# Kernel optimization log

Hardware: AMD Instinct MI355X
Metric: run time of the kernel (lower is better)

The kernel has to match this reference:

```python
import jax, jax.numpy as jnp
import numpy as np

NUM_WIRES = 14
N_LAYERS = 4
BATCH = 128


def _rx_mat(theta):
    # PennyLane RX(t) = [[cos(t/2), -i sin(t/2)], [-i sin(t/2), cos(t/2)]]
    c = jnp.cos(theta / 2).astype(jnp.complex64)
    s = jnp.sin(theta / 2).astype(jnp.complex64)
    row0 = jnp.stack([c, -1j * s], axis=-1)
    row1 = jnp.stack([-1j * s, c], axis=-1)
    return jnp.stack([row0, row1], axis=-2)  # (..., 2, 2)


def _rz_mat(theta):
    # PennyLane RZ(t) = diag(exp(-it/2), exp(it/2))
    e0 = jnp.exp(-1j * theta.astype(jnp.complex64) / 2)
    e1 = jnp.exp(1j * theta.astype(jnp.complex64) / 2)
    z = jnp.zeros_like(e0)
    row0 = jnp.stack([e0, z], axis=-1)
    row1 = jnp.stack([z, e1], axis=-1)
    return jnp.stack([row0, row1], axis=-2)


def _apply_1q(psi, gate, wire):
    # psi: (B, 2, 2, ..., 2); gate: (2,2) shared or (B,2,2) per-sample
    axis = wire + 1
    psi = jnp.moveaxis(psi, axis, -1)
    if gate.ndim == 2:
        psi = psi @ gate.T
    else:
        psi = jnp.einsum('b...j,bij->b...i', psi, gate)
    return jnp.moveaxis(psi, -1, axis)


def _apply_cnot(psi, ctrl, tgt):
    ac, at = ctrl + 1, tgt + 1
    psi0 = jnp.take(psi, 0, axis=ac)
    psi1 = jnp.take(psi, 1, axis=ac)
    at_adj = at - (1 if at > ac else 0)  # target axis shifts after removing ctrl axis
    psi1 = jnp.flip(psi1, axis=at_adj)   # X on target when ctrl=1
    return jnp.stack([psi0, psi1], axis=ac)


def _circuit(x, weights):
    # x: (B, n) real angles; weights: (L, n, 2)
    B = x.shape[0]
    n = NUM_WIRES
    psi = jnp.zeros((B,) + (2,) * n, jnp.complex64)
    psi = psi.at[(slice(None),) + (0,) * n].set(1.0)  # |0...0>
    # data encoding: per-sample RX gates
    for i in range(n):
        psi = _apply_1q(psi, _rx_mat(x[:, i]), i)
    # variational ansatz
    for l in range(N_LAYERS):
        for i in range(n):
            psi = _apply_1q(psi, _rx_mat(weights[l, i, 0]), i)
            psi = _apply_1q(psi, _rz_mat(weights[l, i, 1]), i)
        for i in range(n - 1):
            psi = _apply_cnot(psi, i, i + 1)
        psi = _apply_cnot(psi, n - 1, 0)
    # <Z_i> for every wire
    p = jnp.abs(psi) ** 2  # (B, 2, ..., 2) real
    zs = []
    for i in range(n):
        other = tuple(a for a in range(1, n + 1) if a != i + 1)
        m = jnp.sum(p, axis=other)  # (B, 2)
        zs.append(m[:, 0] - m[:, 1])
    return jnp.stack(zs, axis=-1)  # (B, n)


def setup_inputs() -> dict:
    key = jax.random.key(0)
    k1, k2, k3, k4 = jax.random.split(key, 4)
    states = jax.random.normal(k1, (BATCH, 2 ** NUM_WIRES), dtype=jnp.float32)
    weights = jax.random.normal(k2, (N_LAYERS, NUM_WIRES, 2), dtype=jnp.float32)
    lim = 1.0 / np.sqrt(NUM_WIRES)
    head_w = jax.random.uniform(k3, (1, NUM_WIRES), jnp.float32, -lim, lim)
    head_b = jax.random.uniform(k4, (1,), jnp.float32, -lim, lim)
    return {"states": states, "weights": weights, "head_w": head_w, "head_b": head_b}


def reference(states, weights, head_w, head_b):
    features = jnp.abs(states)[:, :NUM_WIRES]        # (B, n)
    qfeatures = _circuit(features, weights)          # (B, n)
    out = (qfeatures @ head_w.T + head_b)[:, 0]      # (B,)
    return out
```

## Files before the change

kernel.cpp:

```cpp
#include <hip/hip_runtime.h>
#include <math.h>

#define NW 14
#define NSTATE 16384
#define HALF 8192
#define NL 4
#define BATCH 128
#define TPB 1024
#define SHB1 (84 * 1024)
#define SHB2 ((NSTATE + 3 * TPB) * (int)sizeof(float2))


#define B4_  0x201Fu
#define B5_  0x203Fu
#define B12_ 0x3FFFu
#define B13_ 0x1FFFu

#define WAVE_FENCE() __builtin_amdgcn_wave_barrier()

__device__ __forceinline__ unsigned sxmap(unsigned v) {
    unsigned t = v;
    t ^= t >> 1; t ^= t >> 2; t ^= t >> 4; t ^= t >> 8;
    return (t & 0x0FFFu) | ((t & 1u) << 13);
}

__device__ __forceinline__ float2 cmul(float2 u, float2 v) {
    return make_float2(u.x * v.x - u.y * v.y, u.x * v.y + u.y * v.x);
}

__device__ __forceinline__ float4 fused_coef(const float* weights,
                                             const float* states,
                                             int b, int l, int w) {
    float t1 = weights[(l * NW + w) * 2 + 0];
    float t2 = weights[(l * NW + w) * 2 + 1];
    if (l == 0) t1 += fabsf(states[(size_t)b * NSTATE + w]);
    float s, c, sz, cz;
    sincosf(0.5f * t1, &s, &c);
    sincosf(0.5f * t2, &sz, &cz);
    return make_float4(c * cz, -c * sz, -s * sz, -s * cz);
}

template<int N, int M>
__device__ __forceinline__ void gateN(float2* r, float4 g, unsigned s3) {
    const float f = (s3 & (unsigned)M) ? -1.0f : 1.0f;
    g.y *= f;
    g.z *= f;
#pragma unroll
    for (int k = 0; k < N; ++k) {
        if ((k & M) == 0) {
            const float x0 = r[k].x,   y0 = r[k].y;
            const float x1 = r[k|M].x, y1 = r[k|M].y;
            r[k].x   =  g.x*x0 - g.y*y0 + g.z*x1 - g.w*y1;
            r[k].y   =  g.x*y0 + g.y*x0 + g.z*y1 + g.w*x1;
            r[k|M].x = -g.z*x0 - g.w*y0 + g.x*x1 + g.y*y1;
            r[k|M].y = -g.z*y0 + g.w*x0 + g.x*y1 - g.y*x1;
        }
    }
}

template<int J0, int S3SH, int S3MSK>
__device__ __forceinline__ void pass3h(float2* psi, const float4* gc,
                                       unsigned t) {
    const float4 gA = gc[13 - (J0 + 0)];
    const float4 gB = gc[13 - (J0 + 1)];
    const float4 gC = gc[13 - (J0 + 2)];
    const unsigned s3   = (t >> S3SH) & (unsigned)S3MSK;
    const unsigned low  = t & ((1u << J0) - 1u);
    const unsigned high = (t >> J0) << (J0 + 3);
    float2 r[8];
#pragma unroll
    for (int k = 0; k < 8; ++k)
        r[k] = psi[low | (((unsigned)k ^ s3) << J0) | high];
    gateN<8,1>(r, gA, s3);
    gateN<8,2>(r, gB, s3);
    gateN<8,4>(r, gC, s3);
#pragma unroll
    for (int k = 0; k < 8; ++k)
        psi[low | (((unsigned)k ^ s3) << J0) | high] = r[k];
}

template<int J0, int S3SH, int S3MSK>
__device__ __forceinline__ void pass3f(float2* psi, const float4* gc,
                                       unsigned t) {
    const float4 gA = gc[13 - (J0 + 0)];
    const float4 gB = gc[13 - (J0 + 1)];
    const float4 gC = gc[13 - (J0 + 2)];
    const unsigned s3 = (t >> S3SH) & (unsigned)S3MSK;
#pragma unroll
    for (int m = 0; m < 2; ++m) {
        const unsigned x    = t | ((unsigned)m << 10);
        const unsigned low  = x & ((1u << J0) - 1u);
        const unsigned high = (x >> J0) << (J0 + 3);
        float2 r[8];
#pragma unroll
        for (int k = 0; k < 8; ++k)
            r[k] = psi[low | (((unsigned)k ^ s3) << J0) | high];
        gateN<8,1>(r, gA, s3);
        gateN<8,2>(r, gB, s3);
        gateN<8,4>(r, gC, s3);
#pragma unroll
        for (int k = 0; k < 8; ++k)
            psi[low | (((unsigned)k ^ s3) << J0) | high] = r[k];
    }
}

__device__ __forceinline__ void passE(float2* psi, float2* spare,
                                      const float4* gc4, int l, unsigned t) {
    const float4 g1 = gc4[l*NW + 1];
    const float4 g0 = gc4[l*NW + 0];

    unsigned v = t;
    v ^= v >> 1; v ^= v >> 2; v ^= v >> 4; v ^= v >> 8;
    const unsigned Rinv0 = (v & 0x0FFFu) | ((v & 1u) << 13);

    float2 c0[4];
#pragma unroll
    for (int k = 0; k < 4; ++k) c0[k] = psi[t | ((unsigned)k << 12)];
    gateN<4,1>(c0, g1, 0u);
    gateN<4,2>(c0, g0, 0u);
    spare[3*t+0] = c0[1];
    spare[3*t+1] = c0[2];
    spare[3*t+2] = c0[3];
    const float2 keep = c0[0];

    float2 r[12];
#pragma unroll
    for (int m = 1; m < 4; ++m) {
        const unsigned base = t | ((unsigned)m << 10);
#pragma unroll
        for (int k = 0; k < 4; ++k)
            r[(m-1)*4 + k] = psi[base | ((unsigned)k << 12)];
    }
#pragma unroll
    for (int m = 0; m < 3; ++m) {
        gateN<4,1>(r + 4*m, g1, 0u);
        gateN<4,2>(r + 4*m, g0, 0u);
    }

    __syncthreads();

#pragma unroll
    for (int m = 1; m < 4; ++m) {
        const unsigned Rb = Rinv0 ^ ((m & 1) ? 0x27FFu : 0u)
                                  ^ ((m & 2) ? 0x2FFFu : 0u);
#pragma unroll
        for (int k = 0; k < 4; ++k) {
            const unsigned CK = ((k & 1) ? B12_ : 0u) ^ ((k & 2) ? B13_ : 0u);
            psi[Rb ^ CK] = r[(m-1)*4 + k];
        }
    }
    psi[Rinv0]           = keep;
    psi[Rinv0 ^ B12_]    = spare[3*t+0];
    psi[Rinv0 ^ B13_]    = spare[3*t+1];
    psi[Rinv0 ^ 0x2000u] = spare[3*t+2];
}

__device__ __forceinline__ void exit_scatter(const float2* psi,
                                             float2* __restrict__ dst,
                                             float4 g1, unsigned q,
                                             unsigned tid) {
#pragma unroll
    for (int m = 0; m < 4; ++m) {
        const unsigned jc = tid + (unsigned)m * TPB;
        const float2 x0 = psi[jc];
        const float2 x1 = psi[jc | 0x1000u];
        float2 A0, A1;
        A0.x =  g1.x*x0.x - g1.y*x0.y + g1.z*x1.x - g1.w*x1.y;
        A0.y =  g1.x*x0.y + g1.y*x0.x + g1.z*x1.y + g1.w*x1.x;
        A1.x = -g1.z*x0.x - g1.w*x0.y + g1.x*x1.x + g1.y*x1.y;
        A1.y = -g1.z*x0.y + g1.w*x0.x + g1.x*x1.y - g1.y*x1.x;
        const unsigned d0 = sxmap(jc) ^ (q ? 0x1FFFu : 0u);
        dst[d0]           = A0;
        dst[d0 ^ 0x3FFFu] = A1;
    }
}

__global__ __launch_bounds__(TPB) void k_layer1(
    const float* __restrict__ states, const float* __restrict__ weights,
    float2* __restrict__ Sout)
{
    extern __shared__ float2 psi[];
    __shared__ float2 vfac[NW][2];
    __shared__ float2 T1[128];
    __shared__ float2 T2[128];
    __shared__ float4 gc[NW];
    const unsigned gid = blockIdx.x, q = gid >> 7, b = gid & 127u;
    const unsigned tid = threadIdx.x;

    if (tid < NW) {
        float4 g = fused_coef(weights, states, (int)b, 0, (int)tid);
        vfac[tid][0] = make_float2(g.x, g.y);
        vfac[tid][1] = make_float2(-g.z, g.w);
    }
    if (tid >= 64 && tid < 64 + NW)
        gc[tid - 64] = fused_coef(weights, states, (int)b, 1, (int)(tid - 64));
    __syncthreads();
    if (tid < 128) {
        float2 p = make_float2(1.0f, 0.0f);
#pragma unroll
        for (int j = 0; j < 7; ++j)
            p = cmul(p, vfac[13 - j][(tid >> j) & 1u]);
        T1[tid] = p;
    } else if (tid < 256) {
        const unsigned u = tid - 128;
        float2 p = make_float2(1.0f, 0.0f);
#pragma unroll
        for (int j = 7; j < 14; ++j)
            p = cmul(p, vfac[13 - j][(u >> (j - 7)) & 1u]);
        T2[u] = p;
    }
    __syncthreads();

#pragma unroll
    for (int m = 0; m < 8; ++m) {
        const unsigned I  = tid + (unsigned)m * TPB;
        const unsigned If = I | (q << 13);
        const unsigned lo  = (If ^ (If >> 1)) & 0x0FFFu;
        const unsigned y12 = ((If >> 12) ^ (If >> 13) ^ If) & 1u;
        const unsigned y13 = ((If >> 13) ^ If) & 1u;
        const unsigned J = lo | (y12 << 12) | (y13 << 13);
        psi[I] = cmul(T1[J & 127u], T2[J >> 7]);
    }
    __syncthreads();

    pass3h<0, 1, 7>(psi, gc, tid);  WAVE_FENCE();
    pass3h<3, 3, 1>(psi, gc, tid);  WAVE_FENCE();
    pass3h<6, 0, 0>(psi, gc, tid);  __syncthreads();
    pass3h<9, 0, 0>(psi, gc, tid);  __syncthreads();

    exit_scatter(psi, Sout + (size_t)b * NSTATE, gc[1], q, tid);
}

__global__ __launch_bounds__(TPB) void k_rest(
    const float* __restrict__ states, const float* __restrict__ weights,
    const float* __restrict__ head_w, const float* __restrict__ head_b,
    const float2* __restrict__ Sin, float* __restrict__ out)
{
    extern __shared__ float2 dyn[];
    float2* psi   = dyn;
    float2* spare = dyn + NSTATE;
    __shared__ float4 gc4[NL * NW];
    __shared__ float wsum[TPB / 64];
    const unsigned b = blockIdx.x;
    const unsigned tid = threadIdx.x;

    if (tid < NL * NW)
        gc4[tid] = fused_coef(weights, states, (int)b,
                              (int)tid / NW, (int)tid % NW);
    __syncthreads();

    {
        const float4 ge = gc4[1 * NW + 0];
#pragma unroll
        for (int qm = 0; qm < 8; ++qm) {
            const unsigned q = (unsigned)qm >> 2;
            const unsigned m = (unsigned)qm & 3u;
            const float2* src = Sin + (size_t)b * NSTATE + (size_t)q * HALF;
            const unsigned ic = tid + m * TPB;
            const float2 f0 = src[ic];
            const float2 f1 = src[ic ^ 0x1FFFu];
            const unsigned rc = (q ^ ic) & 1u;
            const float aar = ge.x, aai = rc ? -ge.y : ge.y;
            const float bbr = rc ? -ge.z : ge.z, bbi = ge.w;
            float2 oc, op;
            oc.x = aar*f0.x - aai*f0.y + bbr*f1.x - bbi*f1.y;
            oc.y = aar*f0.y + aai*f0.x + bbr*f1.y + bbi*f1.x;
            op.x = aar*f1.x + aai*f1.y - (bbr*f0.x + bbi*f0.y);
            op.y = aar*f1.y - aai*f1.x - (bbr*f0.y - bbi*f0.x);
            psi[(q << 13) | ic]            = oc;
            psi[(q << 13) | (ic ^ 0x1FFFu)] = op;
        }
    }
    __syncthreads();

    pass3f<0, 1, 7>(psi, gc4 + 2 * NW, tid);  WAVE_FENCE();
    pass3f<3, 3, 1>(psi, gc4 + 2 * NW, tid);  WAVE_FENCE();
    pass3f<6, 0, 0>(psi, gc4 + 2 * NW, tid);  __syncthreads();
    pass3f<9, 0, 0>(psi, gc4 + 2 * NW, tid);  __syncthreads();
    passE(psi, spare, gc4, 2, tid);           __syncthreads();

    pass3f<0, 1, 7>(psi, gc4 + 3 * NW, tid);  WAVE_FENCE();
    pass3f<3, 3, 1>(psi, gc4 + 3 * NW, tid);  WAVE_FENCE();
    pass3f<6, 0, 0>(psi, gc4 + 3 * NW, tid);  __syncthreads();
    pass3f<9, 0, 0>(psi, gc4 + 3 * NW, tid);  __syncthreads();

    float hw[NW];
#pragma unroll
    for (int i = 0; i < NW; ++i) hw[i] = head_w[i];
    float H = 0.0f, H12 = 0.0f;
#pragma unroll
    for (int i = 0; i < NW; ++i) H += hw[i];
#pragma unroll
    for (int i = 2; i < NW; ++i) H12 += hw[i];

    const float4 g1 = gc4[3 * NW + 1];
    const float4 g0 = gc4[3 * NW + 0];

    float acc = 0.0f;
#pragma unroll
    for (int m2 = 0; m2 < 4; ++m2) {
        const unsigned base = tid | ((unsigned)m2 << 10);
        float2 r[4];
#pragma unroll
        for (int k = 0; k < 4; ++k)
            r[k] = psi[base | ((unsigned)k << 12)];
        gateN<4,1>(r, g1, 0u);
        gateN<4,2>(r, g0, 0u);
        float A = 0.0f;
        unsigned sfx = 0u;
#pragma unroll
        for (int p = 11; p >= 0; --p) {
            sfx ^= (base >> p) & 1u;
            if (sfx) A += hw[13 - p];
        }
        const unsigned P = sfx;
#pragma unroll
        for (int k = 0; k < 4; ++k) {
            const unsigned u   = ((unsigned)k ^ ((unsigned)k >> 1)) & 1u;
            const unsigned b13 = P ^ ((unsigned)k & 1u);
            float sum = u ? (H12 - A) : A;
            if (u)   sum += hw[1];
            if (b13) sum += hw[0];
            const float cv = H - 2.0f * sum;
            acc += (r[k].x * r[k].x + r[k].y * r[k].y) * cv;
        }
    }
#pragma unroll
    for (int off = 32; off > 0; off >>= 1)
        acc += __shfl_down(acc, off, 64);
    if ((tid & 63u) == 0) wsum[tid >> 6] = acc;
    __syncthreads();
    if (tid == 0) {
        float tot = 0.0f;
#pragma unroll
        for (int i = 0; i < TPB / 64; ++i) tot += wsum[i];
        out[b] = tot + head_b[0];
    }
}

extern "C" void kernel_launch(void* const* d_in, const int* in_sizes, int n_in,
                              void* d_out, int out_size, void* d_ws, size_t ws_size,
                              hipStream_t stream) {
    const float* states  = (const float*)d_in[0];
    const float* weights = (const float*)d_in[1];
    const float* head_w  = (const float*)d_in[2];
    const float* head_b  = (const float*)d_in[3];
    float* out = (float*)d_out;

    float2* SA = (float2*)d_ws;

    k_layer1<<<2 * BATCH, TPB, SHB1, stream>>>(states, weights, SA);
    k_rest  <<<BATCH, TPB, SHB2, stream>>>(states, weights, head_w, head_b,
                                           SA, out);
}
```

Before: 101.1 us.

## Fuse four qubit gates per LDS pass to cut passes and barriers

Replaces the 3-qubit-per-pass shared-memory sweeps (four passes per layer, each thread doing two 8-element groups) with 4-qubit passes. Each thread now loads 16 amplitudes once and applies four gates, so there are three passes per layer and fewer block barriers. Only the first pass keeps an XOR swizzle to avoid bank conflicts. The cost is more registers per thread (16 complex values), which may reduce occupancy, and bank conflicts in the unswizzled passes may change.

```diff
diff --git a/kernel.cpp b/kernel.cpp
--- a/kernel.cpp
+++ b/kernel.cpp
@@ -11,8 +11,6 @@
 #define SHB2 ((NSTATE + 3 * TPB) * (int)sizeof(float2))
 
 
-#define B4_  0x201Fu
-#define B5_  0x203Fu
 #define B12_ 0x3FFFu
 #define B13_ 0x1FFFu
 
@@ -79,29 +77,27 @@
         psi[low | (((unsigned)k ^ s3) << J0) | high] = r[k];
 }
 
-template<int J0, int S3SH, int S3MSK>
-__device__ __forceinline__ void pass3f(float2* psi, const float4* gc,
+template<int J0, bool SWZ>
+__device__ __forceinline__ void pass4f(float2* psi, const float4* gc,
                                        unsigned t) {
     const float4 gA = gc[13 - (J0 + 0)];
     const float4 gB = gc[13 - (J0 + 1)];
     const float4 gC = gc[13 - (J0 + 2)];
-    const unsigned s3 = (t >> S3SH) & (unsigned)S3MSK;
-#pragma unroll
-    for (int m = 0; m < 2; ++m) {
-        const unsigned x    = t | ((unsigned)m << 10);
-        const unsigned low  = x & ((1u << J0) - 1u);
-        const unsigned high = (x >> J0) << (J0 + 3);
-        float2 r[8];
-#pragma unroll
-        for (int k = 0; k < 8; ++k)
-            r[k] = psi[low | (((unsigned)k ^ s3) << J0) | high];
-        gateN<8,1>(r, gA, s3);
-        gateN<8,2>(r, gB, s3);
-        gateN<8,4>(r, gC, s3);
-#pragma unroll
-        for (int k = 0; k < 8; ++k)
-            psi[low | (((unsigned)k ^ s3) << J0) | high] = r[k];
-    }
+    const float4 gD = gc[13 - (J0 + 3)];
+    const unsigned s    = SWZ ? (t & 15u) : 0u;
+    const unsigned low  = t & ((1u << J0) - 1u);
+    const unsigned high = (t >> J0) << (J0 + 4);
+    float2 r[16];
+#pragma unroll
+    for (int k = 0; k < 16; ++k)
+        r[k] = psi[low | (((unsigned)k ^ s) << J0) | high];
+    gateN<16,1>(r, gA, s);
+    gateN<16,2>(r, gB, s);
+    gateN<16,4>(r, gC, s);
+    gateN<16,8>(r, gD, s);
+#pragma unroll
+    for (int k = 0; k < 16; ++k)
+        psi[low | (((unsigned)k ^ s) << J0) | high] = r[k];
 }
 
 __device__ __forceinline__ void passE(float2* psi, float2* spare,
@@ -273,16 +269,14 @@
     }
     __syncthreads();
 
-    pass3f<0, 1, 7>(psi, gc4 + 2 * NW, tid);  WAVE_FENCE();
-    pass3f<3, 3, 1>(psi, gc4 + 2 * NW, tid);  WAVE_FENCE();
-    pass3f<6, 0, 0>(psi, gc4 + 2 * NW, tid);  __syncthreads();
-    pass3f<9, 0, 0>(psi, gc4 + 2 * NW, tid);  __syncthreads();
-    passE(psi, spare, gc4, 2, tid);           __syncthreads();
-
-    pass3f<0, 1, 7>(psi, gc4 + 3 * NW, tid);  WAVE_FENCE();
-    pass3f<3, 3, 1>(psi, gc4 + 3 * NW, tid);  WAVE_FENCE();
-    pass3f<6, 0, 0>(psi, gc4 + 3 * NW, tid);  __syncthreads();
-    pass3f<9, 0, 0>(psi, gc4 + 3 * NW, tid);  __syncthreads();
+    pass4f<0, true >(psi, gc4 + 2 * NW, tid);  WAVE_FENCE();
+    pass4f<4, false>(psi, gc4 + 2 * NW, tid);  __syncthreads();
+    pass4f<8, false>(psi, gc4 + 2 * NW, tid);  __syncthreads();
+    passE(psi, spare, gc4, 2, tid);            __syncthreads();
+
+    pass4f<0, true >(psi, gc4 + 3 * NW, tid);  WAVE_FENCE();
+    pass4f<4, false>(psi, gc4 + 3 * NW, tid);  __syncthreads();
+    pass4f<8, false>(psi, gc4 + 3 * NW, tid);  __syncthreads();
 
     float hw[NW];
 #pragma unroll
```

Measured after the change: 102.2 us (median of 2 runs). About the same (+1.0%).
